# Optimization experiments

Hardware: AMD Instinct MI355X
Metric: run time of the kernel (lower is better)

Reference implementation:

```python
import jax, jax.numpy as jnp
import numpy as np

DIM = 512
HEADS = 8
HEAD_DIM = DIM // HEADS
MLP = 2048
EPS = 1e-5


def _layer_norm(x, g, b):
    mu = jnp.mean(x, axis=-1, keepdims=True)
    var = jnp.var(x, axis=-1, keepdims=True)
    return (x - mu) * jax.lax.rsqrt(var + EPS) * g + b


def setup_inputs() -> dict:
    key = jax.random.key(0)
    ks = jax.random.split(key, 12)
    s = 1.0 / np.sqrt(DIM)
    sm = 1.0 / np.sqrt(MLP)
    return {
        "x": jax.random.normal(ks[0], (2, 4096, DIM), dtype=jnp.float32),
        "Wq": jax.random.normal(ks[1], (DIM, DIM), dtype=jnp.float32) * s,
        "Wk": jax.random.normal(ks[2], (DIM, DIM), dtype=jnp.float32) * s,
        "Wv": jax.random.normal(ks[3], (DIM, DIM), dtype=jnp.float32) * s,
        "Wo": jax.random.normal(ks[4], (DIM, DIM), dtype=jnp.float32) * s,
        "bo": jnp.zeros((DIM,), dtype=jnp.float32),
        "W1": jax.random.normal(ks[5], (DIM, MLP), dtype=jnp.float32) * s,
        "b1": jnp.zeros((MLP,), dtype=jnp.float32),
        "W2": jax.random.normal(ks[6], (MLP, DIM), dtype=jnp.float32) * sm,
        "b2": jnp.zeros((DIM,), dtype=jnp.float32),
        "g1": jnp.ones((DIM,), dtype=jnp.float32),
        "be1": jnp.zeros((DIM,), dtype=jnp.float32),
        "g2": jnp.ones((DIM,), dtype=jnp.float32),
        "be2": jnp.zeros((DIM,), dtype=jnp.float32),
    }


def reference(x, Wq, Wk, Wv, Wo, bo, W1, b1, W2, b2, g1, be1, g2, be2):
    b, n, d = x.shape
    # --- pre-norm multi-head attention ---
    h = _layer_norm(x, g1, be1)
    q = (h @ Wq).reshape(b, n, HEADS, HEAD_DIM).transpose(0, 2, 1, 3)  # [b,h,n,hd]
    k = (h @ Wk).reshape(b, n, HEADS, HEAD_DIM).transpose(0, 2, 1, 3)
    v = (h @ Wv).reshape(b, n, HEADS, HEAD_DIM).transpose(0, 2, 1, 3)
    scores = jnp.einsum("bhqd,bhkd->bhqk", q, k) / np.sqrt(HEAD_DIM)  # [b,h,n,n]
    attn = jax.nn.softmax(scores, axis=-1)
    out = jnp.einsum("bhqk,bhkd->bhqd", attn, v)
    out = out.transpose(0, 2, 1, 3).reshape(b, n, d)
    x = x + out @ Wo + bo
    # --- pre-norm feed-forward ---
    h2 = _layer_norm(x, g2, be2)
    ff = jax.nn.gelu(h2 @ W1 + b1, approximate=False) @ W2 + b2
    return x + ff
```

## Files before the change

kernel.cpp:

```cpp
#include <hip/hip_runtime.h>
#include <math.h>

#define BB   2
#define SEQ  4096
#define DIM  512
#define NH   8
#define HD   64
#define MLPD 2048
#define ROWS (BB*SEQ)
#define SZ   (ROWS*DIM)
#define EPSV 1e-5f

typedef __attribute__((ext_vector_type(8))) short bf16x8;
typedef __attribute__((ext_vector_type(4))) float f32x4;

#if __has_builtin(__builtin_amdgcn_exp2f)
#define EXP2(x) __builtin_amdgcn_exp2f(x)
#else
#define EXP2(x) exp2f(x)
#endif

__device__ __forceinline__ ushort f2bf(float f) {
    unsigned u = __float_as_uint(f);
    u += 0x7fffu + ((u >> 16) & 1u);
    return (ushort)(u >> 16);
}
__device__ __forceinline__ unsigned pack2bf(float a, float b) {
    return (unsigned)f2bf(a) | ((unsigned)f2bf(b) << 16);
}
__device__ __forceinline__ unsigned pack2bf_tr(float a, float b) {
    return (__float_as_uint(a) >> 16) | (__float_as_uint(b) & 0xffff0000u);
}

__device__ __forceinline__ void gload16(const ushort* g, ushort* l) {
    __builtin_amdgcn_global_load_lds(
        (const __attribute__((address_space(1))) unsigned*)g,
        (__attribute__((address_space(3))) unsigned*)l, 16, 0, 0);
}

__global__ __launch_bounds__(128) void ln_kernel(const float* __restrict__ x,
        const float* __restrict__ g, const float* __restrict__ be,
        ushort* __restrict__ out)
{
    int row = blockIdx.x;
    int tid = threadIdx.x;
    const float4 v = ((const float4*)(x + (size_t)row*DIM))[tid];
    float s  = v.x + v.y + v.z + v.w;
    float ss = v.x*v.x + v.y*v.y + v.z*v.z + v.w*v.w;
    #pragma unroll
    for (int off = 32; off > 0; off >>= 1) {
        s  += __shfl_down(s,  off);
        ss += __shfl_down(ss, off);
    }
    __shared__ float red[4];
    if ((tid & 63) == 0) { red[(tid>>6)*2+0] = s; red[(tid>>6)*2+1] = ss; }
    __syncthreads();
    float sum = red[0] + red[2], sumsq = red[1] + red[3];
    float mu  = sum * (1.0f/DIM);
    float var = sumsq * (1.0f/DIM) - mu*mu;
    float rs  = rsqrtf(var + EPSV);
    float4 gv = ((const float4*)g)[tid];
    float4 bv = ((const float4*)be)[tid];
    ushort4 o;
    o.x = f2bf((v.x - mu)*rs*gv.x + bv.x);
    o.y = f2bf((v.y - mu)*rs*gv.y + bv.y);
    o.z = f2bf((v.z - mu)*rs*gv.z + bv.z);
    o.w = f2bf((v.w - mu)*rs*gv.w + bv.w);
    ((ushort4*)(out + (size_t)row*DIM))[tid] = o;
}

__global__ __launch_bounds__(256) void wtrans_kernel(const float* __restrict__ W,
        ushort* __restrict__ Wt, int K, int N)
{
    __shared__ ushort T[64][65];
    int n0 = blockIdx.x*64, k0 = blockIdx.y*64;
    int tid = threadIdx.x;
    #pragma unroll
    for (int p = 0; p < 4; ++p) {
        int r = p*16 + (tid>>4), c = (tid&15)<<2;
        float4 w4 = *(const float4*)(W + (size_t)(k0+r)*N + n0 + c);
        T[c+0][r] = f2bf(w4.x); T[c+1][r] = f2bf(w4.y);
        T[c+2][r] = f2bf(w4.z); T[c+3][r] = f2bf(w4.w);
    }
    __syncthreads();
    #pragma unroll
    for (int p = 0; p < 4; ++p) {
        int n = p*16 + (tid>>4), k = (tid&15)<<2;
        ushort4 o; o.x = T[n][k]; o.y = T[n][k+1]; o.z = T[n][k+2]; o.w = T[n][k+3];
        *(ushort4*)(Wt + (size_t)(n0+n)*K + k0 + k) = o;
    }
}

__global__ __launch_bounds__(256) void wtrans4_kernel(
        const float* __restrict__ W0, const float* __restrict__ W1,
        const float* __restrict__ W2, const float* __restrict__ W3,
        ushort* __restrict__ Wt)
{
    __shared__ ushort T[64][65];
    int z = blockIdx.z;
    const float* W = (z==0) ? W0 : (z==1) ? W1 : (z==2) ? W2 : W3;
    ushort* Wtz = Wt + (size_t)z*512*512;
    int n0 = blockIdx.x*64, k0 = blockIdx.y*64;
    int tid = threadIdx.x;
    #pragma unroll
    for (int p = 0; p < 4; ++p) {
        int r = p*16 + (tid>>4), c = (tid&15)<<2;
        float4 w4 = *(const float4*)(W + (size_t)(k0+r)*512 + n0 + c);
        T[c+0][r] = f2bf(w4.x); T[c+1][r] = f2bf(w4.y);
        T[c+2][r] = f2bf(w4.z); T[c+3][r] = f2bf(w4.w);
    }
    __syncthreads();
    #pragma unroll
    for (int p = 0; p < 4; ++p) {
        int n = p*16 + (tid>>4), k = (tid&15)<<2;
        ushort4 o; o.x = T[n][k]; o.y = T[n][k+1]; o.z = T[n][k+2]; o.w = T[n][k+3];
        *(ushort4*)(Wtz + (size_t)(n0+n)*512 + k0 + k) = o;
    }
}

template<int BM, int NT>
__global__ __launch_bounds__(NT) void gemm_bf16_kernel(
        const ushort* __restrict__ A,
        const ushort* __restrict__ Wta, const ushort* __restrict__ Wtb, const ushort* __restrict__ Wtc,
        const float* __restrict__ bias, const float* __restrict__ resid,
        void* __restrict__ outv, int M, int Nn, int K, int flags)
{
    constexpr int AISS = (BM*4)/NT;
    constexpr int BISS = 256/NT;
    __shared__ ushort As[2][BM*32];
    __shared__ ushort Bs[2][64*32];
    int tid = threadIdx.x;
    int w = tid >> 6, lane = tid & 63, quad = lane >> 4, col = lane & 15;
    int row0 = blockIdx.y * BM, col0 = blockIdx.x * 64;
    int wm0 = w * 32;

    const ushort* Wt; int wcol0, ostride, obase_col;
    float qscale = 1.0f;
    float* outF = nullptr; ushort* outB = nullptr;
    if (flags & 1) {
        int sel = col0 >> 9;
        Wt = (sel == 0) ? Wta : ((sel == 1) ? Wtb : Wtc);
        wcol0 = col0 & 511; ostride = 512; obase_col = wcol0;
        outB = (ushort*)outv + (size_t)sel * ((size_t)M * 512);
        if (sel == 0) qscale = 0.125f * 1.44269504088896f;
        flags |= 16;
    } else {
        Wt = Wta; wcol0 = col0; ostride = Nn; obase_col = col0;
        if (flags & 16) outB = (ushort*)outv; else outF = (float*)outv;
    }

    f32x4 acc[2][4];
    #pragma unroll
    for (int i = 0; i < 2; ++i)
        #pragma unroll
        for (int j = 0; j < 4; ++j) acc[i][j] = (f32x4){0.f,0.f,0.f,0.f};

    const ushort* Ag = A  + (size_t)(row0  + (tid >> 2))*K + ((tid & 3) << 3);
    const ushort* Bg = Wt + (size_t)(wcol0 + (tid >> 2))*K + ((tid & 3) << 3);

    auto issue = [&](ushort* Ad, ushort* Bd, int ko) {
        #pragma unroll
        for (int it = 0; it < AISS; ++it)
            gload16(Ag + ko + (size_t)(it*(NT/4))*K, Ad + it*NT*8 + tid*8);
        #pragma unroll
        for (int it = 0; it < BISS; ++it)
            gload16(Bg + ko + (size_t)(it*(NT/4))*K, Bd + it*NT*8 + tid*8);
    };
    auto compute = [&](const ushort* Ab, const ushort* Bb) {
        bf16x8 af[2], bfr[4];
        #pragma unroll
        for (int i = 0; i < 2; ++i)
            af[i] = *(const bf16x8*)(Ab + (wm0 + i*16 + col)*32 + quad*8);
        #pragma unroll
        for (int j = 0; j < 4; ++j)
            bfr[j] = *(const bf16x8*)(Bb + (j*16 + col)*32 + quad*8);
        #pragma unroll
        for (int i = 0; i < 2; ++i)
            #pragma unroll
            for (int j = 0; j < 4; ++j)
                acc[i][j] = __builtin_amdgcn_mfma_f32_16x16x32_bf16(af[i], bfr[j], acc[i][j], 0, 0, 0);
    };

    int niter = K >> 5;
    issue(As[0], Bs[0], 0);
    for (int i = 0; i < niter; i += 2) {
        __syncthreads();
        if (i + 1 < niter) issue(As[1], Bs[1], (i+1)*32);
        compute(As[0], Bs[0]);
        __syncthreads();
        if (i + 2 < niter) issue(As[0], Bs[0], (i+2)*32);
        compute(As[1], Bs[1]);
    }

    #pragma unroll
    for (int i = 0; i < 2; ++i) {
        #pragma unroll
        for (int r = 0; r < 4; ++r) {
            int row = row0 + wm0 + i*16 + quad*4 + r;
            #pragma unroll
            for (int j = 0; j < 4; ++j) {
                int oc = obase_col + j*16 + col;
                float o = acc[i][j][r] * qscale;
                if (flags & 8) o += bias[oc];
                if (flags & 2) o = 0.5f*o*(1.f + erff(o*0.70710678118654752f));
                if (flags & 4) o += resid[(size_t)row*ostride + oc];
                if (flags & 16) outB[(size_t)row*ostride + oc] = f2bf(o);
                else            outF[(size_t)row*ostride + oc] = o;
            }
        }
    }
}

__global__ __launch_bounds__(256) void vtrans_kernel(const ushort* __restrict__ v,
                                                     ushort* __restrict__ vt)
{
    int tt = blockIdx.x, bh = blockIdx.y;
    int b = bh >> 3, h = bh & 7;
    int tid = threadIdx.x;
    int d = tid >> 2, t0 = (tid & 3) << 4;
    ushort tmp[16];
    #pragma unroll
    for (int i = 0; i < 16; ++i) {
        int kp = t0 + i;
        int korig = ((kp>>5)*2 + ((kp>>2)&1))*16 + ((kp>>3)&3)*4 + (kp&3);
        tmp[i] = v[(size_t)(b*SEQ + tt*64 + korig)*DIM + h*HD + d];
    }
    unsigned u[8];
    #pragma unroll
    for (int j = 0; j < 8; ++j) u[j] = (unsigned)tmp[2*j] | ((unsigned)tmp[2*j+1] << 16);
    ushort* dst = vt + ((size_t)bh*HD + d)*SEQ + tt*64 + t0;
    *(uint4*)(dst)     = make_uint4(u[0],u[1],u[2],u[3]);
    *(uint4*)(dst + 8) = make_uint4(u[4],u[5],u[6],u[7]);
}

__global__ __launch_bounds__(256) void attn_mfma_kernel(
        const ushort* __restrict__ q, const ushort* __restrict__ k,
        const ushort* __restrict__ vt, ushort* __restrict__ out)
{
    __shared__ ushort Kt[2][64][72];
    __shared__ ushort Vt[2][64][72];

    int qt = blockIdx.x, bh = blockIdx.y;
    int b = bh >> 3, h = bh & 7;
    int tid = threadIdx.x;
    int w = tid >> 6, lane = tid & 63;
    int quad = lane >> 4, col = lane & 15;
    int qn0 = qt*128 + w*32;

    bf16x8 aq[2][2];
    #pragma unroll
    for (int mt = 0; mt < 2; ++mt) {
        const ushort* qp = q + (size_t)(b*SEQ + qn0 + mt*16 + col)*DIM + h*HD + quad*8;
        aq[mt][0] = *(const bf16x8*)(qp);
        aq[mt][1] = *(const bf16x8*)(qp + 32);
    }
    const short one_bf = (short)0x3F80;
    const bf16x8 ones = {one_bf,one_bf,one_bf,one_bf,one_bf,one_bf,one_bf,one_bf};

    f32x4 ot[2][4];
    f32x4 ol[2];
    #pragma unroll
    for (int mt = 0; mt < 2; ++mt) {
        ol[mt] = (f32x4){0.f,0.f,0.f,0.f};
        #pragma unroll
        for (int t4 = 0; t4 < 4; ++t4) ot[mt][t4] = (f32x4){0.f,0.f,0.f,0.f};
    }

    int skey = tid >> 2, sd0 = (tid & 3) << 4;
    bf16x8 kr[2], vr[2];
    auto load_tile = [&](int t) {
        const ushort* kp = k + (size_t)(b*SEQ + t*64 + skey)*DIM + h*HD + sd0;
        kr[0] = *(const bf16x8*)(kp);
        kr[1] = *(const bf16x8*)(kp + 8);
        const ushort* vp = vt + ((size_t)bh*HD + skey)*SEQ + t*64 + sd0;
        vr[0] = *(const bf16x8*)(vp);
        vr[1] = *(const bf16x8*)(vp + 8);
    };
    auto store_tile = [&](int p) {
        *(bf16x8*)&Kt[p][skey][sd0]     = kr[0];
        *(bf16x8*)&Kt[p][skey][sd0+8]   = kr[1];
        *(bf16x8*)&Vt[p][skey][sd0]     = vr[0];
        *(bf16x8*)&Vt[p][skey][sd0+8]   = vr[1];
    };

    load_tile(0);
    store_tile(0);
    __syncthreads();

    for (int t = 0; t < SEQ/64; ++t) {
        int p = t & 1;
        if (t + 1 < SEQ/64) load_tile(t + 1);

        f32x4 sc[2][4];
        #pragma unroll
        for (int mt = 0; mt < 2; ++mt)
            #pragma unroll
            for (int t4 = 0; t4 < 4; ++t4) sc[mt][t4] = (f32x4){0.f,0.f,0.f,0.f};
        #pragma unroll
        for (int c = 0; c < 2; ++c) {
            bf16x8 kf[4];
            #pragma unroll
            for (int t4 = 0; t4 < 4; ++t4)
                kf[t4] = *(const bf16x8*)&Kt[p][t4*16 + col][c*32 + quad*8];
            #pragma unroll
            for (int mt = 0; mt < 2; ++mt)
                #pragma unroll
                for (int t4 = 0; t4 < 4; ++t4)
                    sc[mt][t4] = __builtin_amdgcn_mfma_f32_16x16x32_bf16(kf[t4], aq[mt][c], sc[mt][t4], 0, 0, 0);
        }

        union PU { bf16x8 v; uint4 u; };
        PU pb[2][2];
        #pragma unroll
        for (int mt = 0; mt < 2; ++mt)
            #pragma unroll
            for (int c = 0; c < 2; ++c) {
                pb[mt][c].u.x = pack2bf_tr(EXP2(sc[mt][2*c  ][0]), EXP2(sc[mt][2*c  ][1]));
                pb[mt][c].u.y = pack2bf_tr(EXP2(sc[mt][2*c  ][2]), EXP2(sc[mt][2*c  ][3]));
                pb[mt][c].u.z = pack2bf_tr(EXP2(sc[mt][2*c+1][0]), EXP2(sc[mt][2*c+1][1]));
                pb[mt][c].u.w = pack2bf_tr(EXP2(sc[mt][2*c+1][2]), EXP2(sc[mt][2*c+1][3]));
            }

        #pragma unroll
        for (int c = 0; c < 2; ++c) {
            bf16x8 vf[4];
            #pragma unroll
            for (int t4 = 0; t4 < 4; ++t4)
                vf[t4] = *(const bf16x8*)&Vt[p][t4*16 + col][c*32 + quad*8];
            #pragma unroll
            for (int mt = 0; mt < 2; ++mt) {
                #pragma unroll
                for (int t4 = 0; t4 < 4; ++t4)
                    ot[mt][t4] = __builtin_amdgcn_mfma_f32_16x16x32_bf16(vf[t4], pb[mt][c].v, ot[mt][t4], 0, 0, 0);
                ol[mt] = __builtin_amdgcn_mfma_f32_16x16x32_bf16(ones, pb[mt][c].v, ol[mt], 0, 0, 0);
            }
        }

        if (t + 1 < SEQ/64) store_tile(p ^ 1);
        __syncthreads();
    }

    #pragma unroll
    for (int mt = 0; mt < 2; ++mt) {
        float inv = 1.0f / ol[mt][0];
        #pragma unroll
        for (int t4 = 0; t4 < 4; ++t4) {
            ushort4 o4;
            o4.x = f2bf(ot[mt][t4][0] * inv);
            o4.y = f2bf(ot[mt][t4][1] * inv);
            o4.z = f2bf(ot[mt][t4][2] * inv);
            o4.w = f2bf(ot[mt][t4][3] * inv);
            *(ushort4*)(out + (size_t)(b*SEQ + qn0 + mt*16 + col)*DIM + h*HD + t4*16 + quad*4) = o4;
        }
    }
}

extern "C" void kernel_launch(void* const* d_in, const int* in_sizes, int n_in,
                              void* d_out, int out_size, void* d_ws, size_t ws_size,
                              hipStream_t stream)
{
    (void)in_sizes; (void)n_in; (void)out_size; (void)ws_size;
    const float* x   = (const float*)d_in[0];
    const float* Wq  = (const float*)d_in[1];
    const float* Wk  = (const float*)d_in[2];
    const float* Wv  = (const float*)d_in[3];
    const float* Wo  = (const float*)d_in[4];
    const float* bo  = (const float*)d_in[5];
    const float* W1  = (const float*)d_in[6];
    const float* b1  = (const float*)d_in[7];
    const float* W2  = (const float*)d_in[8];
    const float* b2  = (const float*)d_in[9];
    const float* g1  = (const float*)d_in[10];
    const float* be1 = (const float*)d_in[11];
    const float* g2  = (const float*)d_in[12];
    const float* be2 = (const float*)d_in[13];

    ushort* u = (ushort*)d_ws;
    float*  x2    = (float*)u;
    ushort* h     = u + 2*(size_t)SZ;
    ushort* qb    = u + 3*(size_t)SZ;
    ushort* kb    = u + 4*(size_t)SZ;
    ushort* vb    = u + 5*(size_t)SZ;
    ushort* vtb   = u + 6*(size_t)SZ;
    ushort* attnb = u + 7*(size_t)SZ;
    ushort* ff1   = u + 3*(size_t)SZ;
    ushort* wqkv  = u + 8*(size_t)SZ;
    ushort* wto   = wqkv + 3*(size_t)512*512;
    ushort* wt1   = wqkv + 4*(size_t)512*512;
    ushort* wt2   = wt1  + (size_t)512*2048;
    float*  outp  = (float*)d_out;

    wtrans4_kernel<<<dim3(8,8,4), 256, 0, stream>>>(Wq, Wk, Wv, Wo, wqkv);
    wtrans_kernel<<<dim3(32,8), 256, 0, stream>>>(W1, wt1, 512, 2048);
    wtrans_kernel<<<dim3(8,32), 256, 0, stream>>>(W2, wt2, 2048, 512);

    ln_kernel<<<ROWS, 128, 0, stream>>>(x, g1, be1, h);
    gemm_bf16_kernel<128,256><<<dim3(1536/64, ROWS/128), 256, 0, stream>>>(
        h, wqkv, wqkv + (size_t)512*512, wqkv + 2*(size_t)512*512,
        nullptr, nullptr, qb, ROWS, 1536, DIM, 1);
    vtrans_kernel<<<dim3(SEQ/64, BB*NH), 256, 0, stream>>>(vb, vtb);
    attn_mfma_kernel<<<dim3(SEQ/128, BB*NH), 256, 0, stream>>>(qb, kb, vtb, attnb);
    gemm_bf16_kernel<64,128><<<dim3(DIM/64, ROWS/64), 128, 0, stream>>>(
        attnb, wto, wto, wto, bo, x, x2, ROWS, DIM, DIM, 8|4);
    ln_kernel<<<ROWS, 128, 0, stream>>>(x2, g2, be2, h);
    gemm_bf16_kernel<128,256><<<dim3(MLPD/64, ROWS/128), 256, 0, stream>>>(
        h, wt1, wt1, wt1, b1, nullptr, ff1, ROWS, MLPD, DIM, 8|2|16);
    gemm_bf16_kernel<64,128><<<dim3(DIM/64, ROWS/64), 128, 0, stream>>>(
        ff1, wt2, wt2, wt2, b2, x2, outp, ROWS, DIM, MLPD, 8|4);
}
```

Before: 364.9 us.

## Split attention key tile across wave pairs with shared-memory reduction of partial outputs

Each attention block's four waves are regrouped into two query groups of 64 rows, and each pair splits every 64-key tile into two 32-key halves. Each wave now loads half as many K fragments from LDS per tile and reuses them across four query sub-tiles, and V fragments are read for only its 32 keys. The partial O and row-sum accumulators from the two key halves are combined through LDS at the end. This doubles the per-wave accumulator registers, so a launch-bounds occupancy hint of 2 blocks is added, with some risk of register spills.

```diff
diff --git a/kernel.cpp b/kernel.cpp
--- a/kernel.cpp
+++ b/kernel.cpp
@@ -233,37 +233,39 @@
     *(uint4*)(dst + 8) = make_uint4(u[4],u[5],u[6],u[7]);
 }
 
-__global__ __launch_bounds__(256) void attn_mfma_kernel(
+__global__ __launch_bounds__(256, 2) void attn_mfma_kernel(
         const ushort* __restrict__ q, const ushort* __restrict__ k,
         const ushort* __restrict__ vt, ushort* __restrict__ out)
 {
-    __shared__ ushort Kt[2][64][72];
-    __shared__ ushort Vt[2][64][72];
+    __shared__ __align__(16) ushort Kt[2][64][72];
+    __shared__ __align__(16) ushort Vt[2][64][72];
 
     int qt = blockIdx.x, bh = blockIdx.y;
     int b = bh >> 3, h = bh & 7;
     int tid = threadIdx.x;
     int w = tid >> 6, lane = tid & 63;
     int quad = lane >> 4, col = lane & 15;
-    int qn0 = qt*128 + w*32;
-
-    bf16x8 aq[2][2];
-    #pragma unroll
-    for (int mt = 0; mt < 2; ++mt) {
+    int qw = w >> 1, kw = w & 1;
+    int qn0 = qt*128 + qw*64;
+
+    bf16x8 aq[4][2];
+    #pragma unroll
+    for (int mt = 0; mt < 4; ++mt) {
         const ushort* qp = q + (size_t)(b*SEQ + qn0 + mt*16 + col)*DIM + h*HD + quad*8;
         aq[mt][0] = *(const bf16x8*)(qp);
         aq[mt][1] = *(const bf16x8*)(qp + 32);
     }
     const short one_bf = (short)0x3F80;
     const bf16x8 ones = {one_bf,one_bf,one_bf,one_bf,one_bf,one_bf,one_bf,one_bf};
-
-    f32x4 ot[2][4];
-    f32x4 ol[2];
-    #pragma unroll
-    for (int mt = 0; mt < 2; ++mt) {
-        ol[mt] = (f32x4){0.f,0.f,0.f,0.f};
-        #pragma unroll
-        for (int t4 = 0; t4 < 4; ++t4) ot[mt][t4] = (f32x4){0.f,0.f,0.f,0.f};
+    const f32x4 zf = {0.f,0.f,0.f,0.f};
+
+    f32x4 ot[4][4];
+    f32x4 ol[4];
+    #pragma unroll
+    for (int mt = 0; mt < 4; ++mt) {
+        ol[mt] = zf;
+        #pragma unroll
+        for (int t4 = 0; t4 < 4; ++t4) ot[mt][t4] = zf;
     }
 
     int skey = tid >> 2, sd0 = (tid & 3) << 4;
@@ -287,70 +289,84 @@
     store_tile(0);
     __syncthreads();
 
+    int krow0 = kw << 5;
     for (int t = 0; t < SEQ/64; ++t) {
         int p = t & 1;
         if (t + 1 < SEQ/64) load_tile(t + 1);
 
-        f32x4 sc[2][4];
-        #pragma unroll
-        for (int mt = 0; mt < 2; ++mt)
+        bf16x8 kf0[2], kf1[2];
+        #pragma unroll
+        for (int kb = 0; kb < 2; ++kb) {
+            const ushort* kbp = &Kt[p][krow0 + kb*16 + col][quad*8];
+            kf0[kb] = *(const bf16x8*)(kbp);
+            kf1[kb] = *(const bf16x8*)(kbp + 32);
+        }
+        f32x4 sc[4][2];
+        #pragma unroll
+        for (int mt = 0; mt < 4; ++mt)
             #pragma unroll
-            for (int t4 = 0; t4 < 4; ++t4) sc[mt][t4] = (f32x4){0.f,0.f,0.f,0.f};
-        #pragma unroll
-        for (int c = 0; c < 2; ++c) {
-            bf16x8 kf[4];
+            for (int kb = 0; kb < 2; ++kb) {
+                sc[mt][kb] = __builtin_amdgcn_mfma_f32_16x16x32_bf16(kf0[kb], aq[mt][0], zf, 0, 0, 0);
+                sc[mt][kb] = __builtin_amdgcn_mfma_f32_16x16x32_bf16(kf1[kb], aq[mt][1], sc[mt][kb], 0, 0, 0);
+            }
+
+        union PU { bf16x8 v; uint4 u; };
+        PU pb[4];
+        #pragma unroll
+        for (int mt = 0; mt < 4; ++mt) {
+            pb[mt].u.x = pack2bf_tr(EXP2(sc[mt][0][0]), EXP2(sc[mt][0][1]));
+            pb[mt].u.y = pack2bf_tr(EXP2(sc[mt][0][2]), EXP2(sc[mt][0][3]));
+            pb[mt].u.z = pack2bf_tr(EXP2(sc[mt][1][0]), EXP2(sc[mt][1][1]));
+            pb[mt].u.w = pack2bf_tr(EXP2(sc[mt][1][2]), EXP2(sc[mt][1][3]));
+        }
+
+        bf16x8 vf[4];
+        #pragma unroll
+        for (int t4 = 0; t4 < 4; ++t4)
+            vf[t4] = *(const bf16x8*)&Vt[p][t4*16 + col][krow0 + quad*8];
+        #pragma unroll
+        for (int mt = 0; mt < 4; ++mt) {
             #pragma unroll
             for (int t4 = 0; t4 < 4; ++t4)
-                kf[t4] = *(const bf16x8*)&Kt[p][t4*16 + col][c*32 + quad*8];
-            #pragma unroll
-            for (int mt = 0; mt < 2; ++mt)
-                #pragma unroll
-                for (int t4 = 0; t4 < 4; ++t4)
-                    sc[mt][t4] = __builtin_amdgcn_mfma_f32_16x16x32_bf16(kf[t4], aq[mt][c], sc[mt][t4], 0, 0, 0);
-        }
-
-        union PU { bf16x8 v; uint4 u; };
-        PU pb[2][2];
-        #pragma unroll
-        for (int mt = 0; mt < 2; ++mt)
-            #pragma unroll
-            for (int c = 0; c < 2; ++c) {
-                pb[mt][c].u.x = pack2bf_tr(EXP2(sc[mt][2*c  ][0]), EXP2(sc[mt][2*c  ][1]));
-                pb[mt][c].u.y = pack2bf_tr(EXP2(sc[mt][2*c  ][2]), EXP2(sc[mt][2*c  ][3]));
-                pb[mt][c].u.z = pack2bf_tr(EXP2(sc[mt][2*c+1][0]), EXP2(sc[mt][2*c+1][1]));
-                pb[mt][c].u.w = pack2bf_tr(EXP2(sc[mt][2*c+1][2]), EXP2(sc[mt][2*c+1][3]));
-            }
-
-        #pragma unroll
-        for (int c = 0; c < 2; ++c) {
-            bf16x8 vf[4];
-            #pragma unroll
-            for (int t4 = 0; t4 < 4; ++t4)
-                vf[t4] = *(const bf16x8*)&Vt[p][t4*16 + col][c*32 + quad*8];
-            #pragma unroll
-            for (int mt = 0; mt < 2; ++mt) {
-                #pragma unroll
-                for (int t4 = 0; t4 < 4; ++t4)
-                    ot[mt][t4] = __builtin_amdgcn_mfma_f32_16x16x32_bf16(vf[t4], pb[mt][c].v, ot[mt][t4], 0, 0, 0);
-                ol[mt] = __builtin_amdgcn_mfma_f32_16x16x32_bf16(ones, pb[mt][c].v, ol[mt], 0, 0, 0);
-            }
+                ot[mt][t4] = __builtin_amdgcn_mfma_f32_16x16x32_bf16(vf[t4], pb[mt].v, ot[mt][t4], 0, 0, 0);
+            ol[mt] = __builtin_amdgcn_mfma_f32_16x16x32_bf16(ones, pb[mt].v, ol[mt], 0, 0, 0);
         }
 
         if (t + 1 < SEQ/64) store_tile(p ^ 1);
         __syncthreads();
     }
 
-    #pragma unroll
-    for (int mt = 0; mt < 2; ++mt) {
-        float inv = 1.0f / ol[mt][0];
+    f32x4* redA = (f32x4*)Kt;
+    f32x4* redB = (f32x4*)Vt;
+    int rbase = ((qw << 6) + lane) * 9;
+    if (kw) {
         #pragma unroll
         for (int t4 = 0; t4 < 4; ++t4) {
-            ushort4 o4;
-            o4.x = f2bf(ot[mt][t4][0] * inv);
-            o4.y = f2bf(ot[mt][t4][1] * inv);
-            o4.z = f2bf(ot[mt][t4][2] * inv);
-            o4.w = f2bf(ot[mt][t4][3] * inv);
-            *(ushort4*)(out + (size_t)(b*SEQ + qn0 + mt*16 + col)*DIM + h*HD + t4*16 + quad*4) = o4;
+            redA[rbase + t4]     = ot[0][t4];
+            redA[rbase + 4 + t4] = ot[1][t4];
+            redB[rbase + t4]     = ot[2][t4];
+            redB[rbase + 4 + t4] = ot[3][t4];
+        }
+        redA[rbase + 8] = (f32x4){ol[0][0], ol[1][0], ol[2][0], ol[3][0]};
+    }
+    __syncthreads();
+    if (!kw) {
+        f32x4 olp = redA[rbase + 8];
+        #pragma unroll
+        for (int mt = 0; mt < 4; ++mt) {
+            float inv = 1.0f / (ol[mt][0] + olp[mt]);
+            #pragma unroll
+            for (int t4 = 0; t4 < 4; ++t4) {
+                f32x4 r = (mt < 2) ? redA[rbase + mt*4 + t4]
+                                   : redB[rbase + (mt-2)*4 + t4];
+                f32x4 o = ot[mt][t4] + r;
+                ushort4 o4;
+                o4.x = f2bf(o[0] * inv);
+                o4.y = f2bf(o[1] * inv);
+                o4.z = f2bf(o[2] * inv);
+                o4.w = f2bf(o[3] * inv);
+                *(ushort4*)(out + (size_t)(b*SEQ + qn0 + mt*16 + col)*DIM + h*HD + t4*16 + quad*4) = o4;
+            }
         }
     }
 }
```

New measurement: 349.1 us. -4.3%, faster.
